# Kernel tuning notes

Hardware: AMD Instinct MI355X
Metric: run time of the kernel (lower is better)

## Reference

```python
import jax, jax.numpy as jnp
import numpy as np
import math

B, S, E, H = 4, 2048, 512, 8
D = E // H

def setup_inputs() -> dict:
    key = jax.random.key(0)
    ks = jax.random.split(key, 12)
    inp = {
        'query': jax.random.normal(ks[0], (B, S, E), jnp.float32),
        'key': jax.random.normal(ks[1], (B, S, E), jnp.float32),
        'value': jax.random.normal(ks[2], (B, S, E), jnp.float32),
        'mask': jnp.ones((B, S), jnp.int32),
        'position_bias': jax.random.normal(ks[3], (H, S, S), jnp.float32) * 0.02,
        'Wq': jax.random.normal(ks[4], (E, E), jnp.float32) * 0.02,
        'bq': jnp.zeros((E,), jnp.float32),
        'Wk': jax.random.normal(ks[5], (E, E), jnp.float32) * 0.02,
        'bk': jnp.zeros((E,), jnp.float32),
        'Wv': jax.random.normal(ks[6], (E, E), jnp.float32) * 0.02,
        'bv': jnp.zeros((E,), jnp.float32),
        'Wo': jax.random.normal(ks[7], (E, E), jnp.float32) * 0.02,
        'bo': jnp.zeros((E,), jnp.float32),
    }
    return inp

def reference(query, key, value, mask, position_bias, Wq, bq, Wk, bk, Wv, bv, Wo, bo):
    scale = math.sqrt(D)
    # torch Linear: x @ W.T + b
    Q = (query @ Wq.T + bq).reshape(B, S, H, D).transpose(0, 2, 1, 3)  # bhsd
    K = (key @ Wk.T + bk).reshape(B, S, H, D).transpose(0, 2, 1, 3)
    V = (value @ Wv.T + bv).reshape(B, S, H, D).transpose(0, 2, 1, 3)
    scores = jnp.einsum('bhqd,bhkd->bhqk', Q, K) / scale
    scores = scores + position_bias[None]
    causal = jnp.triu(jnp.ones((S, S), bool), k=1)  # True above diagonal
    scores = jnp.where(causal[None, None], -jnp.inf, scores)
    scores = jnp.where(mask[:, None, None, :] == 0, -jnp.inf, scores)
    attn = jax.nn.softmax(scores, axis=-1)  # dropout is eval no-op
    ctx = jnp.einsum('bhqk,bhkd->bqhd', attn, V).reshape(B, S, E)
    out = ctx @ Wo.T + bo
    return out, attn
```

## Files before the change

kernel.cpp:

```cpp
#include <hip/hip_runtime.h>

typedef __attribute__((ext_vector_type(8))) __bf16 bf16x8;
typedef __attribute__((ext_vector_type(4))) float f32x4;
typedef __attribute__((ext_vector_type(4))) unsigned short u16x4;
typedef unsigned short u16;

#define OFF_QB   0L
#define OFF_KB   4194304L
#define OFF_VB   8388608L
#define OFF_WQ   12582912L
#define OFF_WK   12845056L
#define OFF_WV   13107200L
#define OFF_WO   13369344L
#define OFF_QS   13631488L
#define OFF_KS   17825792L
#define OFF_VT   22020096L
#define OFF_CTX  26214400L
#define WS_NEEDED_U16 30408704L

static __device__ __forceinline__ u16 f2bf(float f) {
  union { float f; unsigned u; } v; v.f = f;
  unsigned r = v.u + 0x7FFFu + ((v.u >> 16) & 1u);
  return (u16)(r >> 16);
}

static __device__ __forceinline__ f32x4 mfma16(bf16x8 a, bf16x8 b, f32x4 c) {
  return __builtin_amdgcn_mfma_f32_16x16x32_bf16(a, b, c, 0, 0, 0);
}

__global__ __launch_bounds__(256) void k_cvt(
    const float* __restrict__ q, const float* __restrict__ k, const float* __restrict__ v,
    const float* __restrict__ wq, const float* __restrict__ wk, const float* __restrict__ wv,
    const float* __restrict__ wo, u16* __restrict__ ws0) {
  long i = ((long)blockIdx.x * 256 + threadIdx.x) * 4;
  const float* src; u16* dst; long off;
  if (i < 12582912L) {
    int which = (int)(i >> 22); off = i & 4194303L;
    src = which == 0 ? q : which == 1 ? k : v;
    dst = ws0 + (long)which * 4194304L;
  } else {
    long j = i - 12582912L;
    int which = (int)(j >> 18); off = j & 262143L;
    src = which == 0 ? wq : which == 1 ? wk : which == 2 ? wv : wo;
    dst = ws0 + 12582912L + (long)which * 262144L;
  }
  float4 f = *(const float4*)(src + off);
  u16x4 o; o.x = f2bf(f.x); o.y = f2bf(f.y); o.z = f2bf(f.z); o.w = f2bf(f.w);
  *(u16x4*)(dst + off) = o;
}

__global__ __launch_bounds__(256) void k_proj_qk(
    const u16* __restrict__ ws0, const float* __restrict__ bq, const float* __restrict__ bk) {
  const int wv  = threadIdx.x >> 6;
  const int lane = threadIdx.x & 63;
  const int r16 = lane & 15, g8 = (lane >> 4) * 8, rq = (lane >> 4) * 4;
  const int t0 = blockIdx.x * 64 + wv * 16;
  const int e0 = blockIdx.y * 64;
  const int z  = blockIdx.z;
  const u16* xb = ws0 + (z == 0 ? OFF_QB : OFF_KB);
  const u16* wb = ws0 + (z == 0 ? OFF_WQ : OFF_WK);
  const float* bias = (z == 0) ? bq : bk;
  u16* dst = (u16*)ws0 + (z == 0 ? OFF_QS : OFF_KS);
  const float scl = (z == 0) ? 0.125f : 1.0f;

  f32x4 acc[4] = {};
  const u16* arow = xb + (long)(t0 + r16) * 512 + g8;
  for (int f = 0; f < 512; f += 32) {
    bf16x8 a = *(const bf16x8*)(arow + f);
#pragma unroll
    for (int nt = 0; nt < 4; ++nt) {
      bf16x8 bfr = *(const bf16x8*)(wb + (long)(e0 + nt * 16 + r16) * 512 + f + g8);
      acc[nt] = mfma16(a, bfr, acc[nt]);
    }
  }
#pragma unroll
  for (int nt = 0; nt < 4; ++nt) {
    int e = e0 + nt * 16 + r16;
    float bb = bias[e];
    int h = e >> 6, d = e & 63;
#pragma unroll
    for (int r = 0; r < 4; ++r) {
      int t = t0 + rq + r;
      int b = t >> 11, s = t & 2047;
      float val = (acc[nt][r] + bb) * scl;
      dst[((long)(b * 8 + h) * 2048 + s) * 64 + d] = f2bf(val);
    }
  }
}

__global__ __launch_bounds__(256) void k_proj_v(
    const u16* __restrict__ ws0, const float* __restrict__ bv) {
  const int wv  = threadIdx.x >> 6;
  const int lane = threadIdx.x & 63;
  const int r16 = lane & 15, g8 = (lane >> 4) * 8, rq = (lane >> 4) * 4;
  const int e0 = blockIdx.x * 64 + wv * 16;
  const int t0 = blockIdx.y * 64;
  const u16* xb = ws0 + OFF_VB;
  const u16* wb = ws0 + OFF_WV;
  u16* vt = (u16*)ws0 + OFF_VT;

  f32x4 acc[4] = {};
  const u16* arow = wb + (long)(e0 + r16) * 512 + g8;
  for (int f = 0; f < 512; f += 32) {
    bf16x8 a = *(const bf16x8*)(arow + f);
#pragma unroll
    for (int nt = 0; nt < 4; ++nt) {
      bf16x8 bfr = *(const bf16x8*)(xb + (long)(t0 + nt * 16 + r16) * 512 + f + g8);
      acc[nt] = mfma16(a, bfr, acc[nt]);
    }
  }
#pragma unroll
  for (int r = 0; r < 4; ++r) {
    int e = e0 + rq + r;
    float bb = bv[e];
    int h = e >> 6, d = e & 63;
#pragma unroll
    for (int nt = 0; nt < 4; ++nt) {
      int t = t0 + nt * 16 + r16;
      int b = t >> 11, s = t & 2047;
      vt[((long)((b * 8 + h) * 64 + d)) * 2048 + s] = f2bf(acc[nt][r] + bb);
    }
  }
}

__global__ __launch_bounds__(256) void k_attn(
    const u16* __restrict__ ws0, const float* __restrict__ pos_bias,
    const int* __restrict__ mask, float* __restrict__ attn_out, u16* __restrict__ ctx) {
  __shared__ __align__(16) u16 p_st[4][16][40];
  const int tid = threadIdx.x;
  const int w = tid >> 6, lane = tid & 63;
  const int r16 = lane & 15, g = lane >> 4;
  const int g8 = g * 8, rq = g * 4;
  const int bh = blockIdx.y;
  const int b = bh >> 3, h = bh & 7;
  const int qbw = blockIdx.x * 4 + w;
  const u16* Qs = ws0 + OFF_QS + (long)bh * (2048 * 64);
  const u16* Ks = ws0 + OFF_KS + (long)bh * (2048 * 64);
  const u16* VT = ws0 + OFF_VT + (long)bh * (64 * 2048);
  const int* maskb = mask + b * 2048;
  const float NEG = -1e30f;
  const float L2E = 1.4426950408889634f;

  for (int qsel = 0; qsel < 2; ++qsel) {
    const int qb = qsel ? (127 - qbw) : qbw;
    const int q0 = qb * 16;
    const int ntiles = qb + 1;
    const int kend = ntiles * 16;
    bf16x8 qf0 = *(const bf16x8*)(Qs + (long)(q0 + r16) * 64 + g8);
    bf16x8 qf1 = *(const bf16x8*)(Qs + (long)(q0 + r16) * 64 + 32 + g8);
    const float* brow = pos_bias + ((long)h * 2048 + q0 + rq) * 2048;

    float l[4] = {0.f, 0.f, 0.f, 0.f};
    for (int tb = 0; tb < ntiles; tb += 4) {
#pragma unroll
      for (int t = 0; t < 4; ++t) {
        int ti = tb + t;
        if (ti >= ntiles) break;
        int kcol = ti * 16 + r16;
        bf16x8 kf0 = *(const bf16x8*)(Ks + (long)kcol * 64 + g8);
        bf16x8 kf1 = *(const bf16x8*)(Ks + (long)kcol * 64 + 32 + g8);
        f32x4 s = {};
        s = mfma16(qf0, kf0, s);
        s = mfma16(qf1, kf1, s);
        bool mz = (maskb[kcol] == 0);
#pragma unroll
        for (int r = 0; r < 4; ++r) {
          float sv = s[r] + brow[(long)r * 2048 + kcol];
          if (kcol > q0 + rq + r || mz) sv = NEG;
          l[r] += __expf(sv);
        }
      }
    }
    float cc[4];
#pragma unroll
    for (int r = 0; r < 4; ++r) {
#pragma unroll
      for (int off = 1; off < 16; off <<= 1) l[r] += __shfl_xor(l[r], off);
      cc[r] = -__log2f(l[r]);
    }

    f32x4 cacc[4] = {};
    float* arow = attn_out + ((long)bh * 2048 + q0) * 2048;
    const int ngrp = (ntiles + 1) >> 1;
    for (int gi = 0; gi < ngrp; ++gi) {
      const int t0i = 2 * gi, t1i = 2 * gi + 1;
      const bool have1 = (t1i < ntiles);
      float p0[4], p1[4];
      {
        int kcol = t0i * 16 + r16;
        bf16x8 kf0 = *(const bf16x8*)(Ks + (long)kcol * 64 + g8);
        bf16x8 kf1 = *(const bf16x8*)(Ks + (long)kcol * 64 + 32 + g8);
        f32x4 s = {};
        s = mfma16(qf0, kf0, s);
        s = mfma16(qf1, kf1, s);
        bool mz = (maskb[kcol] == 0);
#pragma unroll
        for (int r = 0; r < 4; ++r) {
          float sv = s[r] + brow[(long)r * 2048 + kcol];
          if (kcol > q0 + rq + r || mz) sv = NEG;
          float pv = exp2f(fmaf(sv, L2E, cc[r]));
          p0[r] = pv;
          __builtin_nontemporal_store(pv, &arow[(long)(rq + r) * 2048 + kcol]);
        }
      }
      if (have1) {
        int kcol = t1i * 16 + r16;
        bf16x8 kf0 = *(const bf16x8*)(Ks + (long)kcol * 64 + g8);
        bf16x8 kf1 = *(const bf16x8*)(Ks + (long)kcol * 64 + 32 + g8);
        f32x4 s = {};
        s = mfma16(qf0, kf0, s);
        s = mfma16(qf1, kf1, s);
        bool mz = (maskb[kcol] == 0);
#pragma unroll
        for (int r = 0; r < 4; ++r) {
          float sv = s[r] + brow[(long)r * 2048 + kcol];
          if (kcol > q0 + rq + r || mz) sv = NEG;
          float pv = exp2f(fmaf(sv, L2E, cc[r]));
          p1[r] = pv;
          __builtin_nontemporal_store(pv, &arow[(long)(rq + r) * 2048 + kcol]);
        }
      } else {
#pragma unroll
        for (int r = 0; r < 4; ++r) p1[r] = 0.0f;
      }
#pragma unroll
      for (int r = 0; r < 4; ++r) {
        p_st[w][rq + r][r16]      = f2bf(p0[r]);
        p_st[w][rq + r][16 + r16] = f2bf(p1[r]);
      }
      int tb2 = (g8 < 16) ? t0i : (have1 ? t1i : t0i);
      const u16* vcol = VT + tb2 * 16 + (g8 & 15);
      bf16x8 pa = *(const bf16x8*)&p_st[w][r16][g8];
#pragma unroll
      for (int dt = 0; dt < 4; ++dt) {
        bf16x8 vf = *(const bf16x8*)(vcol + (long)(dt * 16 + r16) * 2048);
        cacc[dt] = mfma16(pa, vf, cacc[dt]);
      }
    }

    for (int rr = 0; rr < 16; ++rr) {
      float* rowp = arow + (long)rr * 2048;
      for (int k2 = kend + lane * 4; k2 < 2048; k2 += 256) {
        f32x4 z = {0.f, 0.f, 0.f, 0.f};
        __builtin_nontemporal_store(z, (f32x4*)(rowp + k2));
      }
    }

#pragma unroll
    for (int dt = 0; dt < 4; ++dt) {
#pragma unroll
      for (int r = 0; r < 4; ++r) {
        ctx[(long)(b * 2048 + q0 + rq + r) * 512 + h * 64 + dt * 16 + r16] =
            f2bf(cacc[dt][r]);
      }
    }
  }
}

__global__ __launch_bounds__(256) void k_oproj(
    const u16* __restrict__ ws0, const float* __restrict__ bo, float* __restrict__ out) {
  const int wv  = threadIdx.x >> 6;
  const int lane = threadIdx.x & 63;
  const int r16 = lane & 15, g8 = (lane >> 4) * 8, rq = (lane >> 4) * 4;
  const int t0 = blockIdx.x * 64 + wv * 16;
  const int e0 = blockIdx.y * 64;
  const u16* ctx = ws0 + OFF_CTX;
  const u16* wb  = ws0 + OFF_WO;
  f32x4 acc[4] = {};
  const u16* arow = ctx + (long)(t0 + r16) * 512 + g8;
  for (int f = 0; f < 512; f += 32) {
    bf16x8 a = *(const bf16x8*)(arow + f);
#pragma unroll
    for (int nt = 0; nt < 4; ++nt) {
      bf16x8 bfr = *(const bf16x8*)(wb + (long)(e0 + nt * 16 + r16) * 512 + f + g8);
      acc[nt] = mfma16(a, bfr, acc[nt]);
    }
  }
#pragma unroll
  for (int nt = 0; nt < 4; ++nt) {
    int e = e0 + nt * 16 + r16;
    float bb = bo[e];
#pragma unroll
    for (int r = 0; r < 4; ++r) {
      out[(long)(t0 + rq + r) * 512 + e] = acc[nt][r] + bb;
    }
  }
}

extern "C" void kernel_launch(void* const* d_in, const int* in_sizes, int n_in,
                              void* d_out, int out_size, void* d_ws, size_t ws_size,
                              hipStream_t stream) {
  if (ws_size < (size_t)WS_NEEDED_U16 * sizeof(u16)) return;
  const float* query = (const float*)d_in[0];
  const float* key   = (const float*)d_in[1];
  const float* value = (const float*)d_in[2];
  const int*   mask  = (const int*)d_in[3];
  const float* pbias = (const float*)d_in[4];
  const float* Wq = (const float*)d_in[5];
  const float* bq = (const float*)d_in[6];
  const float* Wk = (const float*)d_in[7];
  const float* bk = (const float*)d_in[8];
  const float* Wv = (const float*)d_in[9];
  const float* bv = (const float*)d_in[10];
  const float* Wo = (const float*)d_in[11];
  const float* bo = (const float*)d_in[12];
  float* out  = (float*)d_out;
  float* attn = out + 4194304L;
  u16* ws0 = (u16*)d_ws;

  k_cvt<<<13312, 256, 0, stream>>>(query, key, value, Wq, Wk, Wv, Wo, ws0);
  k_proj_qk<<<dim3(128, 8, 2), 256, 0, stream>>>(ws0, bq, bk);
  k_proj_v<<<dim3(8, 128), 256, 0, stream>>>(ws0, bv);
  k_attn<<<dim3(16, 32), 256, 0, stream>>>(ws0, pbias, mask, attn, (u16*)ws0 + OFF_CTX);
  k_oproj<<<dim3(128, 8), 256, 0, stream>>>(ws0, bo, out);
}
```

Measured before the change: 408.1 us.

## Split attention key tiles across four waves with shared-memory reductions

Each block used to give four independent 16-row query blocks to its four waves. Now all four waves of a block work on the same query block and split its key tiles among themselves. The row sums and context partials are reduced through shared memory, and the grid grows from 16 to 64 blocks along x. The log2(e) factor is folded into the Q projection scale and the causal test only runs on the diagonal tile. This is meant to raise parallelism and balance work for the long causal rows, at the cost of extra syncthreads and shared-memory reduction traffic.

```diff
diff --git a/kernel.cpp b/kernel.cpp
--- a/kernel.cpp
+++ b/kernel.cpp
@@ -61,7 +61,7 @@
   const u16* wb = ws0 + (z == 0 ? OFF_WQ : OFF_WK);
   const float* bias = (z == 0) ? bq : bk;
   u16* dst = (u16*)ws0 + (z == 0 ? OFF_QS : OFF_KS);
-  const float scl = (z == 0) ? 0.125f : 1.0f;
+  const float scl = (z == 0) ? 0.125f * 1.4426950408889634f : 1.0f;
 
   f32x4 acc[4] = {};
   const u16* arow = xb + (long)(t0 + r16) * 512 + g8;
@@ -127,22 +127,28 @@
     const u16* __restrict__ ws0, const float* __restrict__ pos_bias,
     const int* __restrict__ mask, float* __restrict__ attn_out, u16* __restrict__ ctx) {
   __shared__ __align__(16) u16 p_st[4][16][40];
+  __shared__ float red_l[4][16];
+  __shared__ __align__(16) float cred[4][16][68];
+
   const int tid = threadIdx.x;
   const int w = tid >> 6, lane = tid & 63;
   const int r16 = lane & 15, g = lane >> 4;
   const int g8 = g * 8, rq = g * 4;
   const int bh = blockIdx.y;
   const int b = bh >> 3, h = bh & 7;
-  const int qbw = blockIdx.x * 4 + w;
+  const int pair = blockIdx.x;
   const u16* Qs = ws0 + OFF_QS + (long)bh * (2048 * 64);
   const u16* Ks = ws0 + OFF_KS + (long)bh * (2048 * 64);
   const u16* VT = ws0 + OFF_VT + (long)bh * (64 * 2048);
   const int* maskb = mask + b * 2048;
   const float NEG = -1e30f;
   const float L2E = 1.4426950408889634f;
+  bool dg[4];
+#pragma unroll
+  for (int r = 0; r < 4; ++r) dg[r] = (r16 > rq + r);
 
   for (int qsel = 0; qsel < 2; ++qsel) {
-    const int qb = qsel ? (127 - qbw) : qbw;
+    const int qb = qsel ? (127 - pair) : pair;
     const int q0 = qb * 16;
     const int ntiles = qb + 1;
     const int kend = ntiles * 16;
@@ -151,71 +157,76 @@
     const float* brow = pos_bias + ((long)h * 2048 + q0 + rq) * 2048;
 
     float l[4] = {0.f, 0.f, 0.f, 0.f};
-    for (int tb = 0; tb < ntiles; tb += 4) {
-#pragma unroll
-      for (int t = 0; t < 4; ++t) {
-        int ti = tb + t;
-        if (ti >= ntiles) break;
-        int kcol = ti * 16 + r16;
+    for (int ti = w; ti < ntiles; ti += 4) {
+      int kcol = ti * 16 + r16;
+      bf16x8 kf0 = *(const bf16x8*)(Ks + (long)kcol * 64 + g8);
+      bf16x8 kf1 = *(const bf16x8*)(Ks + (long)kcol * 64 + 32 + g8);
+      f32x4 s = {};
+      s = mfma16(qf0, kf0, s);
+      s = mfma16(qf1, kf1, s);
+      bool mz = (maskb[kcol] == 0);
+      bool edge = (ti == qb);
+#pragma unroll
+      for (int r = 0; r < 4; ++r) {
+        float sv = fmaf(brow[(long)r * 2048 + kcol], L2E, s[r]);
+        if (mz || (edge && dg[r])) sv = NEG;
+        l[r] += exp2f(sv);
+      }
+    }
+#pragma unroll
+    for (int r = 0; r < 4; ++r)
+#pragma unroll
+      for (int off = 1; off < 16; off <<= 1) l[r] += __shfl_xor(l[r], off);
+    if (r16 == 0) {
+#pragma unroll
+      for (int r = 0; r < 4; ++r) red_l[w][rq + r] = l[r];
+    }
+    __syncthreads();
+    float cc[4];
+#pragma unroll
+    for (int r = 0; r < 4; ++r) {
+      float ls = red_l[0][rq + r] + red_l[1][rq + r] + red_l[2][rq + r] + red_l[3][rq + r];
+      cc[r] = -__log2f(ls);
+    }
+
+    f32x4 cacc[4] = {};
+    float* arow = attn_out + ((long)bh * 2048 + q0) * 2048;
+    for (int ta = w; ta < ntiles; ta += 8) {
+      const int tb = ta + 4;
+      const bool have1 = (tb < ntiles);
+      float p0[4], p1[4];
+      {
+        int kcol = ta * 16 + r16;
         bf16x8 kf0 = *(const bf16x8*)(Ks + (long)kcol * 64 + g8);
         bf16x8 kf1 = *(const bf16x8*)(Ks + (long)kcol * 64 + 32 + g8);
         f32x4 s = {};
         s = mfma16(qf0, kf0, s);
         s = mfma16(qf1, kf1, s);
         bool mz = (maskb[kcol] == 0);
+        bool edge = (ta == qb);
 #pragma unroll
         for (int r = 0; r < 4; ++r) {
-          float sv = s[r] + brow[(long)r * 2048 + kcol];
-          if (kcol > q0 + rq + r || mz) sv = NEG;
-          l[r] += __expf(sv);
+          float sv = fmaf(brow[(long)r * 2048 + kcol], L2E, s[r]);
+          if (mz || (edge && dg[r])) sv = NEG;
+          float pv = exp2f(sv + cc[r]);
+          p0[r] = pv;
+          __builtin_nontemporal_store(pv, &arow[(long)(rq + r) * 2048 + kcol]);
         }
       }
-    }
-    float cc[4];
-#pragma unroll
-    for (int r = 0; r < 4; ++r) {
-#pragma unroll
-      for (int off = 1; off < 16; off <<= 1) l[r] += __shfl_xor(l[r], off);
-      cc[r] = -__log2f(l[r]);
-    }
-
-    f32x4 cacc[4] = {};
-    float* arow = attn_out + ((long)bh * 2048 + q0) * 2048;
-    const int ngrp = (ntiles + 1) >> 1;
-    for (int gi = 0; gi < ngrp; ++gi) {
-      const int t0i = 2 * gi, t1i = 2 * gi + 1;
-      const bool have1 = (t1i < ntiles);
-      float p0[4], p1[4];
-      {
-        int kcol = t0i * 16 + r16;
+      if (have1) {
+        int kcol = tb * 16 + r16;
         bf16x8 kf0 = *(const bf16x8*)(Ks + (long)kcol * 64 + g8);
         bf16x8 kf1 = *(const bf16x8*)(Ks + (long)kcol * 64 + 32 + g8);
         f32x4 s = {};
         s = mfma16(qf0, kf0, s);
         s = mfma16(qf1, kf1, s);
         bool mz = (maskb[kcol] == 0);
+        bool edge = (tb == qb);
 #pragma unroll
         for (int r = 0; r < 4; ++r) {
-          float sv = s[r] + brow[(long)r * 2048 + kcol];
-          if (kcol > q0 + rq + r || mz) sv = NEG;
-          float pv = exp2f(fmaf(sv, L2E, cc[r]));
-          p0[r] = pv;
-          __builtin_nontemporal_store(pv, &arow[(long)(rq + r) * 2048 + kcol]);
-        }
-      }
-      if (have1) {
-        int kcol = t1i * 16 + r16;
-        bf16x8 kf0 = *(const bf16x8*)(Ks + (long)kcol * 64 + g8);
-        bf16x8 kf1 = *(const bf16x8*)(Ks + (long)kcol * 64 + 32 + g8);
-        f32x4 s = {};
-        s = mfma16(qf0, kf0, s);
-        s = mfma16(qf1, kf1, s);
-        bool mz = (maskb[kcol] == 0);
-#pragma unroll
-        for (int r = 0; r < 4; ++r) {
-          float sv = s[r] + brow[(long)r * 2048 + kcol];
-          if (kcol > q0 + rq + r || mz) sv = NEG;
-          float pv = exp2f(fmaf(sv, L2E, cc[r]));
+          float sv = fmaf(brow[(long)r * 2048 + kcol], L2E, s[r]);
+          if (mz || (edge && dg[r])) sv = NEG;
+          float pv = exp2f(sv + cc[r]);
           p1[r] = pv;
           __builtin_nontemporal_store(pv, &arow[(long)(rq + r) * 2048 + kcol]);
         }
@@ -228,8 +239,8 @@
         p_st[w][rq + r][r16]      = f2bf(p0[r]);
         p_st[w][rq + r][16 + r16] = f2bf(p1[r]);
       }
-      int tb2 = (g8 < 16) ? t0i : (have1 ? t1i : t0i);
-      const u16* vcol = VT + tb2 * 16 + (g8 & 15);
+      int tsel = (g < 2) ? ta : (have1 ? tb : ta);
+      const u16* vcol = VT + tsel * 16 + (g8 & 15);
       bf16x8 pa = *(const bf16x8*)&p_st[w][r16][g8];
 #pragma unroll
       for (int dt = 0; dt < 4; ++dt) {
@@ -237,23 +248,32 @@
         cacc[dt] = mfma16(pa, vf, cacc[dt]);
       }
     }
-
-    for (int rr = 0; rr < 16; ++rr) {
+#pragma unroll
+    for (int dt = 0; dt < 4; ++dt)
+#pragma unroll
+      for (int r = 0; r < 4; ++r)
+        cred[w][rq + r][dt * 16 + r16] = cacc[dt][r];
+
+    for (int rr = w; rr < 16; rr += 4) {
       float* rowp = arow + (long)rr * 2048;
       for (int k2 = kend + lane * 4; k2 < 2048; k2 += 256) {
         f32x4 z = {0.f, 0.f, 0.f, 0.f};
         __builtin_nontemporal_store(z, (f32x4*)(rowp + k2));
       }
     }
-
-#pragma unroll
-    for (int dt = 0; dt < 4; ++dt) {
-#pragma unroll
-      for (int r = 0; r < 4; ++r) {
-        ctx[(long)(b * 2048 + q0 + rq + r) * 512 + h * 64 + dt * 16 + r16] =
-            f2bf(cacc[dt][r]);
-      }
-    }
+    __syncthreads();
+    {
+      int row = tid >> 4, c0 = (tid & 15) * 4;
+      u16x4 o;
+#pragma unroll
+      for (int j = 0; j < 4; ++j) {
+        float sum = cred[0][row][c0 + j] + cred[1][row][c0 + j] +
+                    cred[2][row][c0 + j] + cred[3][row][c0 + j];
+        o[j] = f2bf(sum);
+      }
+      *(u16x4*)&ctx[(long)(b * 2048 + q0 + row) * 512 + h * 64 + c0] = o;
+    }
+    __syncthreads();
   }
 }
 
@@ -311,6 +331,6 @@
   k_cvt<<<13312, 256, 0, stream>>>(query, key, value, Wq, Wk, Wv, Wo, ws0);
   k_proj_qk<<<dim3(128, 8, 2), 256, 0, stream>>>(ws0, bq, bk);
   k_proj_v<<<dim3(8, 128), 256, 0, stream>>>(ws0, bv);
-  k_attn<<<dim3(16, 32), 256, 0, stream>>>(ws0, pbias, mask, attn, (u16*)ws0 + OFF_CTX);
+  k_attn<<<dim3(64, 32), 256, 0, stream>>>(ws0, pbias, mask, attn, (u16*)ws0 + OFF_CTX);
   k_oproj<<<dim3(128, 8), 256, 0, stream>>>(ws0, bo, out);
 }
```

Measured after the change: 429.8 us. +5.3%, slower.
